# Optimization experiments

Measured on AMD Instinct MI355X. Metric: run time of the kernel, lower is better.

## Reference

```python
import math
import jax, jax.numpy as jnp
import numpy as np

B, N, F, K = 4, 4096, 128, 32
EPS = 1e-8  # tsl.epsilon
TEMP0, TEMP_DECAY = 1.0, 0.99995


def setup_inputs() -> dict:
    key = jax.random.key(0)
    k1, k2, k3, k4 = jax.random.split(key, 4)
    emb = jax.random.normal(k1, (B, N, F), dtype=jnp.float32)
    adj = jax.random.uniform(k2, (B, N, N), dtype=jnp.float32)
    logits_param = jax.random.normal(k3, (N, K), dtype=jnp.float32)
    u = jax.random.uniform(k4, (B, N, K), dtype=jnp.float32, minval=1e-9, maxval=1.0)
    gumbel_noise = -jnp.log(-jnp.log(u))
    return {"emb": emb, "adj": adj, "logits_param": logits_param, "gumbel_noise": gumbel_noise}


def reference(emb, adj, logits_param, gumbel_noise):
    # temp decays on each get_temp() call in training mode (called twice per forward)
    t1 = max(TEMP0 * TEMP_DECAY, 0.05)
    t2 = max(t1 * TEMP_DECAY, 0.05)

    # ---- gumbel-softmax hard sample with straight-through estimator ----
    y_soft = jax.nn.softmax(logits_param[None] / t1 + gumbel_noise, axis=-1)  # [B,N,K]
    y_hard = jax.nn.one_hot(jnp.argmax(y_soft, axis=-1), K, dtype=y_soft.dtype)
    s_sample = jax.lax.stop_gradient(y_hard - y_soft) + y_soft + EPS  # [B,N,K]

    # ---- soft assignment for regularizers (unbatched [N,K]) ----
    s_soft = jax.nn.softmax(logits_param / t2, axis=-1)  # [N,K]

    # mincut_num = trace(s^T A s) per batch, without forming [K,K]
    As = jnp.einsum('bnm,mk->bnk', adj, s_soft)            # [B,N,K]
    mincut_num = jnp.einsum('nk,bnk->b', s_soft, As)       # [B]
    # mincut_den = trace(s^T D s): D is diag(deg) -> O(N*K) instead of diag_embed
    d_flat = adj.sum(axis=-1)                              # [B,N]
    mincut_den = jnp.einsum('bn,nk,nk->b', d_flat, s_soft, s_soft)
    mincut_loss = -jnp.mean(mincut_num / mincut_den)

    ss = s_soft.T @ s_soft                                 # [K,K]
    ortho_loss = jnp.linalg.norm(ss / jnp.linalg.norm(ss) - jnp.eye(K, dtype=ss.dtype) / math.sqrt(K))

    # ---- pooling ----
    out_emb = jnp.einsum('bnk,bnf->bkf', s_sample, emb)    # [B,K,F]
    As2 = jnp.einsum('bnm,bml->bnl', adj, s_sample)        # [B,N,K]
    out_adj = jnp.einsum('bnk,bnl->bkl', s_sample, As2)    # [B,K,K]

    out_adj = out_adj * (1.0 - jnp.eye(K, dtype=out_adj.dtype))  # zero diagonal
    d = jnp.sqrt(out_adj.sum(axis=-1, keepdims=True)) + EPS
    out_adj = out_adj / d / jnp.swapaxes(d, -1, -2)

    return out_emb, out_adj, s_sample, mincut_loss, ortho_loss
```

## Files before the change

kernel.cpp:

```cpp
#include <hip/hip_runtime.h>
#include <hip/hip_bf16.h>
#include <math.h>

#define B_ 4
#define N_ 4096
#define F_ 128
#define K_ 32
#define EPS_ 1e-8f

typedef __attribute__((ext_vector_type(8))) __bf16 bf16x8;
typedef __attribute__((ext_vector_type(4))) float f32x4;

#define WS_SSOFT 0
#define WS_SQ    131072
#define WS_SS    135168
#define WS_NUM   136192
#define WS_DEN   136196
#define WS_OADJ  136200
#define WS_WF    140296
#define WS_H     664584

__global__ void k_ssoft(const float* __restrict__ logits, float* __restrict__ s_soft,
                        float* __restrict__ sq, float* __restrict__ ss, float t2) {
  __shared__ float sl[64][33];
  int t = threadIdx.x;
  int rowbase = blockIdx.x * 64;
  if (t < 64) {
    int n = rowbase + t;
    float z[32];
    float mx = -1e30f;
    for (int k = 0; k < 32; ++k) { z[k] = logits[n*32+k] / t2; mx = fmaxf(mx, z[k]); }
    float s = 0.f;
    for (int k = 0; k < 32; ++k) { z[k] = expf(z[k]-mx); s += z[k]; }
    float sqa = 0.f;
    for (int k = 0; k < 32; ++k) {
      float v = z[k] / s;
      s_soft[n*32+k] = v;
      sl[t][k] = v;
      sqa += v*v;
    }
    sq[n] = sqa;
  }
  __syncthreads();
  for (int pp = 0; pp < 4; ++pp) {
    int p = pp*256 + t;
    int k = p >> 5, l = p & 31;
    float a = 0.f;
    for (int r = 0; r < 64; ++r) a += sl[r][k]*sl[r][l];
    atomicAdd(&ss[p], a);
  }
}

__global__ void k_gumbel(const float* __restrict__ logits, const float* __restrict__ gum,
                         float* __restrict__ s_sample, int* __restrict__ h, float t1) {
  int i = blockIdx.x*256 + threadIdx.x;
  int n = i & (N_-1);
  float z[32];
  float mx = -1e30f;
  for (int k = 0; k < 32; ++k) { z[k] = logits[n*32+k]/t1 + gum[(size_t)i*32+k]; mx = fmaxf(mx, z[k]); }
  float s = 0.f;
  for (int k = 0; k < 32; ++k) { z[k] = expf(z[k]-mx); s += z[k]; }
  int am = 0; float best = -1.f;
  for (int k = 0; k < 32; ++k) { z[k] = z[k]/s; if (z[k] > best) { best = z[k]; am = k; } }
  for (int k = 0; k < 32; ++k) {
    float yh = (k==am) ? 1.f : 0.f;
    s_sample[(size_t)i*32+k] = (yh - z[k]) + z[k] + EPS_;
  }
  h[i] = am;
}

__global__ void k_wfrag(const float* __restrict__ s_soft, const int* __restrict__ h,
                        bf16x8* __restrict__ wf) {
  int i = blockIdx.x*256 + threadIdx.x;
  int lane = i & 63;
  int c = (i >> 6) & 3;
  int tt = (i >> 8) & 127;
  int b = i >> 15;
  int col = c*16 + (lane & 15);
  int m0 = tt*32 + (lane >> 4)*8;
  bf16x8 v;
  if (col < 32) {
    for (int j = 0; j < 8; ++j) v[j] = (__bf16)s_soft[(m0+j)*32 + col];
  } else {
    int cc = col - 32;
    for (int j = 0; j < 8; ++j) v[j] = (__bf16)((h[b*N_ + m0 + j] == cc) ? 1.f : 0.f);
  }
  wf[i] = v;
}

__launch_bounds__(256, 2)
__global__ void k_gemm(const float* __restrict__ adj, const bf16x8* __restrict__ wf,
                       const float* __restrict__ s_soft, const float* __restrict__ sq,
                       const int* __restrict__ h, float* __restrict__ num,
                       float* __restrict__ den, float* __restrict__ oadj) {
  __shared__ float oal[1024];
  __shared__ float rn[4], rd[4];
  int t = threadIdx.x;
  int w = t >> 6, l = t & 63;
  int lr = l & 15, lhi = l >> 4;
  int bid = blockIdx.x;
  int sp = bid & 3, r = (bid >> 2) & 31, b = bid >> 7;

  for (int i = t; i < 1024; i += 256) oal[i] = 0.f;
  __syncthreads();

  int row0 = r*128 + w*32;
  int m0 = sp*1024;
  const float* adjb = adj + (size_t)b*N_*N_;
  const float* arow0 = adjb + (size_t)(row0 + lr)*N_ + m0 + lhi*8;
  const float* arow1 = arow0 + (size_t)16*N_;
  const bf16x8* wfb = wf + ((size_t)b*128 + (m0 >> 5))*256 + l;

  f32x4 acc[2][4];
  for (int i = 0; i < 2; ++i)
    for (int j = 0; j < 4; ++j) acc[i][j] = (f32x4){0.f,0.f,0.f,0.f};

  for (int t32 = 0; t32 < 32; ++t32) {
    float4 a0 = *(const float4*)(arow0);
    float4 a1 = *(const float4*)(arow0 + 4);
    float4 a2 = *(const float4*)(arow1);
    float4 a3 = *(const float4*)(arow1 + 4);
    bf16x8 bf0 = wfb[0], bf1 = wfb[64], bf2 = wfb[128], bf3 = wfb[192];
    bf16x8 af0, af1;
    af0[0]=(__bf16)a0.x; af0[1]=(__bf16)a0.y; af0[2]=(__bf16)a0.z; af0[3]=(__bf16)a0.w;
    af0[4]=(__bf16)a1.x; af0[5]=(__bf16)a1.y; af0[6]=(__bf16)a1.z; af0[7]=(__bf16)a1.w;
    af1[0]=(__bf16)a2.x; af1[1]=(__bf16)a2.y; af1[2]=(__bf16)a2.z; af1[3]=(__bf16)a2.w;
    af1[4]=(__bf16)a3.x; af1[5]=(__bf16)a3.y; af1[6]=(__bf16)a3.z; af1[7]=(__bf16)a3.w;
    acc[0][0] = __builtin_amdgcn_mfma_f32_16x16x32_bf16(af0, bf0, acc[0][0], 0, 0, 0);
    acc[0][1] = __builtin_amdgcn_mfma_f32_16x16x32_bf16(af0, bf1, acc[0][1], 0, 0, 0);
    acc[0][2] = __builtin_amdgcn_mfma_f32_16x16x32_bf16(af0, bf2, acc[0][2], 0, 0, 0);
    acc[0][3] = __builtin_amdgcn_mfma_f32_16x16x32_bf16(af0, bf3, acc[0][3], 0, 0, 0);
    acc[1][0] = __builtin_amdgcn_mfma_f32_16x16x32_bf16(af1, bf0, acc[1][0], 0, 0, 0);
    acc[1][1] = __builtin_amdgcn_mfma_f32_16x16x32_bf16(af1, bf1, acc[1][1], 0, 0, 0);
    acc[1][2] = __builtin_amdgcn_mfma_f32_16x16x32_bf16(af1, bf2, acc[1][2], 0, 0, 0);
    acc[1][3] = __builtin_amdgcn_mfma_f32_16x16x32_bf16(af1, bf3, acc[1][3], 0, 0, 0);
    arow0 += 32; arow1 += 32; wfb += 256;
  }

  float numacc = 0.f, denacc = 0.f;
  for (int rt = 0; rt < 2; ++rt) {
    int rbase = row0 + rt*16 + lhi*4;
    for (int i = 0; i < 4; ++i) {
      int row = rbase + i;
      float sqv = sq[row];
      int hv = h[b*N_ + row];
      numacc += acc[rt][0][i] * s_soft[row*32 + lr];
      numacc += acc[rt][1][i] * s_soft[row*32 + 16 + lr];
      float v2 = acc[rt][2][i], v3 = acc[rt][3][i];
      denacc += (v2 + v3) * sqv;
      atomicAdd(&oal[hv*32 + lr], v2);
      atomicAdd(&oal[hv*32 + 16 + lr], v3);
    }
  }
  for (int off = 32; off; off >>= 1) {
    numacc += __shfl_down(numacc, off);
    denacc += __shfl_down(denacc, off);
  }
  if (l == 0) { rn[w] = numacc; rd[w] = denacc; }
  __syncthreads();
  if (t == 0) {
    atomicAdd(&num[b], rn[0]+rn[1]+rn[2]+rn[3]);
    atomicAdd(&den[b], rd[0]+rd[1]+rd[2]+rd[3]);
  }
  for (int i = t; i < 1024; i += 256) atomicAdd(&oadj[b*1024 + i], oal[i]);
}

__global__ void k_outemb(const float* __restrict__ emb, const int* __restrict__ h,
                         float* __restrict__ out_emb) {
  __shared__ float accl[32*128];
  int t = threadIdx.x;
  for (int i = t; i < 4096; i += 256) accl[i] = 0.f;
  __syncthreads();
  int b = blockIdx.x >> 5;
  int n0 = (blockIdx.x & 31) * 128;
  int f = t & 127, rr = t >> 7;
  for (int it = 0; it < 64; ++it) {
    int n = n0 + it*2 + rr;
    float v = emb[((size_t)b*N_ + n)*F_ + f];
    int hv = h[b*N_ + n];
    atomicAdd(&accl[hv*128 + f], v);
  }
  __syncthreads();
  for (int i = t; i < 4096; i += 256) atomicAdd(&out_emb[b*4096 + i], accl[i]);
}

__global__ void k_final(const float* __restrict__ num, const float* __restrict__ den,
                        const float* __restrict__ oadj, const float* __restrict__ ss,
                        float* __restrict__ dout) {
  __shared__ float dsh[128];
  __shared__ float red[256];
  int t = threadIdx.x;
  if (t < 128) {
    int b = t >> 5, k = t & 31;
    float s = 0.f;
    for (int l = 0; l < 32; ++l) if (l != k) s += oadj[b*1024 + k*32 + l];
    dsh[t] = sqrtf(s) + EPS_;
  }
  __syncthreads();
  for (int i = t; i < 4096; i += 256) {
    int b = i >> 10, k = (i >> 5) & 31, l = i & 31;
    float v = (k == l) ? 0.f : oadj[i] / (dsh[b*32+k] * dsh[b*32+l]);
    dout[16384 + i] = v;
  }
  float a = 0.f;
  for (int i = t; i < 1024; i += 256) { float v = ss[i]; a += v*v; }
  red[t] = a; __syncthreads();
  for (int s2 = 128; s2; s2 >>= 1) { if (t < s2) red[t] += red[t+s2]; __syncthreads(); }
  float fro = sqrtf(red[0]);
  __syncthreads();
  float c = 0.f;
  float inv = 1.f / fro;
  float dk = (float)(1.0 / sqrt(32.0));
  for (int i = t; i < 1024; i += 256) {
    int k = i >> 5, l = i & 31;
    float v = ss[i]*inv - ((k == l) ? dk : 0.f);
    c += v*v;
  }
  red[t] = c; __syncthreads();
  for (int s2 = 128; s2; s2 >>= 1) { if (t < s2) red[t] += red[t+s2]; __syncthreads(); }
  if (t == 0) {
    dout[544769] = sqrtf(red[0]);
    float s = 0.f;
    for (int b = 0; b < 4; ++b) s += num[b]/den[b];
    dout[544768] = -s*0.25f;
  }
}

extern "C" void kernel_launch(void* const* d_in, const int* in_sizes, int n_in,
                              void* d_out, int out_size, void* d_ws, size_t ws_size,
                              hipStream_t stream) {
  const float* emb    = (const float*)d_in[0];
  const float* adj    = (const float*)d_in[1];
  const float* logits = (const float*)d_in[2];
  const float* gum    = (const float*)d_in[3];
  float* out = (float*)d_out;
  float* ws  = (float*)d_ws;

  float t1 = 0.99995f;
  float t2 = (float)(0.99995 * 0.99995);

  float* s_soft = ws + WS_SSOFT;
  float* sq     = ws + WS_SQ;
  float* ss     = ws + WS_SS;
  float* num    = ws + WS_NUM;
  float* den    = ws + WS_DEN;
  float* oadj   = ws + WS_OADJ;
  bf16x8* wf    = (bf16x8*)(ws + WS_WF);
  int* hbuf     = (int*)(ws + WS_H);

  hipMemsetAsync(ss, 0, 5128 * sizeof(float), stream);
  hipMemsetAsync(out, 0, 16384 * sizeof(float), stream);

  k_ssoft <<<64, 256, 0, stream>>>(logits, s_soft, sq, ss, t2);
  k_gumbel<<<64, 256, 0, stream>>>(logits, gum, out + 20480, hbuf, t1);
  k_wfrag <<<512, 256, 0, stream>>>(s_soft, hbuf, wf);
  k_gemm  <<<512, 256, 0, stream>>>(adj, wf, s_soft, sq, hbuf, num, den, oadj);
  k_outemb<<<128, 256, 0, stream>>>(emb, hbuf, out);
  k_final <<<1, 256, 0, stream>>>(num, den, oadj, ss, out);
}
```

Baseline: 473.4 us.

## Split GEMM K-dimension finer, double-buffer adj loads, replace atomics with partial reductions

The adjacency GEMM now splits the reduction dimension eight ways instead of four (1024 blocks), raises launch bounds to four blocks per SM, and software-pipelines the adj loads with a two-stage register double buffer using nontemporal loads. Global atomics for num/den, out_adj and out_emb are replaced by per-block partial outputs that a new reduce kernel and the final kernel sum. This is meant to increase memory-level parallelism on the bandwidth-bound 268MB adj stream and to remove atomic contention and the output memset. The cost is extra workspace traffic for the partials and one more kernel launch.

```diff
diff --git a/kernel.cpp b/kernel.cpp
--- a/kernel.cpp
+++ b/kernel.cpp
@@ -11,14 +11,15 @@
 typedef __attribute__((ext_vector_type(8))) __bf16 bf16x8;
 typedef __attribute__((ext_vector_type(4))) float f32x4;
 
-#define WS_SSOFT 0
-#define WS_SQ    131072
-#define WS_SS    135168
-#define WS_NUM   136192
-#define WS_DEN   136196
-#define WS_OADJ  136200
-#define WS_WF    140296
-#define WS_H     664584
+#define WS_SSOFT   0
+#define WS_SQ      131072
+#define WS_SS      135168
+#define WS_WF      136192
+#define WS_OADJP   660480
+#define WS_NUMDEN  1709056
+#define WS_PEMB    1711104
+#define WS_OADJ    2235392
+#define WS_H       2239488
 
 __global__ void k_ssoft(const float* __restrict__ logits, float* __restrict__ s_soft,
                         float* __restrict__ sq, float* __restrict__ ss, float t2) {
@@ -88,68 +89,81 @@
   wf[i] = v;
 }
 
-__launch_bounds__(256, 2)
+#define CVT8(dst, va, vb) { dst[0]=(__bf16)va[0]; dst[1]=(__bf16)va[1]; dst[2]=(__bf16)va[2]; dst[3]=(__bf16)va[3]; \
+                            dst[4]=(__bf16)vb[0]; dst[5]=(__bf16)vb[1]; dst[6]=(__bf16)vb[2]; dst[7]=(__bf16)vb[3]; }
+
+#define MFMA8(A0,A1,A2,A3,W0,W1,W2,W3) { \
+  bf16x8 af0, af1; CVT8(af0, A0, A1); CVT8(af1, A2, A3); \
+  acc00 = __builtin_amdgcn_mfma_f32_16x16x32_bf16(af0, W0, acc00, 0, 0, 0); \
+  acc01 = __builtin_amdgcn_mfma_f32_16x16x32_bf16(af0, W1, acc01, 0, 0, 0); \
+  acc02 = __builtin_amdgcn_mfma_f32_16x16x32_bf16(af0, W2, acc02, 0, 0, 0); \
+  acc03 = __builtin_amdgcn_mfma_f32_16x16x32_bf16(af0, W3, acc03, 0, 0, 0); \
+  acc10 = __builtin_amdgcn_mfma_f32_16x16x32_bf16(af1, W0, acc10, 0, 0, 0); \
+  acc11 = __builtin_amdgcn_mfma_f32_16x16x32_bf16(af1, W1, acc11, 0, 0, 0); \
+  acc12 = __builtin_amdgcn_mfma_f32_16x16x32_bf16(af1, W2, acc12, 0, 0, 0); \
+  acc13 = __builtin_amdgcn_mfma_f32_16x16x32_bf16(af1, W3, acc13, 0, 0, 0); }
+
+#define NT(p) __builtin_nontemporal_load((const f32x4*)(p))
+
+__launch_bounds__(256, 4)
 __global__ void k_gemm(const float* __restrict__ adj, const bf16x8* __restrict__ wf,
                        const float* __restrict__ s_soft, const float* __restrict__ sq,
-                       const int* __restrict__ h, float* __restrict__ num,
-                       float* __restrict__ den, float* __restrict__ oadj) {
+                       const int* __restrict__ h, float* __restrict__ numden_p,
+                       float* __restrict__ oadjp) {
   __shared__ float oal[1024];
   __shared__ float rn[4], rd[4];
   int t = threadIdx.x;
   int w = t >> 6, l = t & 63;
   int lr = l & 15, lhi = l >> 4;
   int bid = blockIdx.x;
-  int sp = bid & 3, r = (bid >> 2) & 31, b = bid >> 7;
+  int sp = bid & 7, r = (bid >> 3) & 31, b = bid >> 8;
 
   for (int i = t; i < 1024; i += 256) oal[i] = 0.f;
   __syncthreads();
 
   int row0 = r*128 + w*32;
-  int m0 = sp*1024;
-  const float* adjb = adj + (size_t)b*N_*N_;
-  const float* arow0 = adjb + (size_t)(row0 + lr)*N_ + m0 + lhi*8;
-  const float* arow1 = arow0 + (size_t)16*N_;
-  const bf16x8* wfb = wf + ((size_t)b*128 + (m0 >> 5))*256 + l;
-
-  f32x4 acc[2][4];
-  for (int i = 0; i < 2; ++i)
-    for (int j = 0; j < 4; ++j) acc[i][j] = (f32x4){0.f,0.f,0.f,0.f};
-
-  for (int t32 = 0; t32 < 32; ++t32) {
-    float4 a0 = *(const float4*)(arow0);
-    float4 a1 = *(const float4*)(arow0 + 4);
-    float4 a2 = *(const float4*)(arow1);
-    float4 a3 = *(const float4*)(arow1 + 4);
-    bf16x8 bf0 = wfb[0], bf1 = wfb[64], bf2 = wfb[128], bf3 = wfb[192];
-    bf16x8 af0, af1;
-    af0[0]=(__bf16)a0.x; af0[1]=(__bf16)a0.y; af0[2]=(__bf16)a0.z; af0[3]=(__bf16)a0.w;
-    af0[4]=(__bf16)a1.x; af0[5]=(__bf16)a1.y; af0[6]=(__bf16)a1.z; af0[7]=(__bf16)a1.w;
-    af1[0]=(__bf16)a2.x; af1[1]=(__bf16)a2.y; af1[2]=(__bf16)a2.z; af1[3]=(__bf16)a2.w;
-    af1[4]=(__bf16)a3.x; af1[5]=(__bf16)a3.y; af1[6]=(__bf16)a3.z; af1[7]=(__bf16)a3.w;
-    acc[0][0] = __builtin_amdgcn_mfma_f32_16x16x32_bf16(af0, bf0, acc[0][0], 0, 0, 0);
-    acc[0][1] = __builtin_amdgcn_mfma_f32_16x16x32_bf16(af0, bf1, acc[0][1], 0, 0, 0);
-    acc[0][2] = __builtin_amdgcn_mfma_f32_16x16x32_bf16(af0, bf2, acc[0][2], 0, 0, 0);
-    acc[0][3] = __builtin_amdgcn_mfma_f32_16x16x32_bf16(af0, bf3, acc[0][3], 0, 0, 0);
-    acc[1][0] = __builtin_amdgcn_mfma_f32_16x16x32_bf16(af1, bf0, acc[1][0], 0, 0, 0);
-    acc[1][1] = __builtin_amdgcn_mfma_f32_16x16x32_bf16(af1, bf1, acc[1][1], 0, 0, 0);
-    acc[1][2] = __builtin_amdgcn_mfma_f32_16x16x32_bf16(af1, bf2, acc[1][2], 0, 0, 0);
-    acc[1][3] = __builtin_amdgcn_mfma_f32_16x16x32_bf16(af1, bf3, acc[1][3], 0, 0, 0);
-    arow0 += 32; arow1 += 32; wfb += 256;
+  int m0 = sp*512;
+  const float* pa0 = adj + (size_t)b*N_*N_ + (size_t)(row0 + lr)*N_ + m0 + lhi*8;
+  const float* pa1 = pa0 + (size_t)16*N_;
+  const bf16x8* pw = wf + ((size_t)b*128 + (m0 >> 5))*256 + l;
+
+  f32x4 acc00 = {0,0,0,0}, acc01 = {0,0,0,0}, acc02 = {0,0,0,0}, acc03 = {0,0,0,0};
+  f32x4 acc10 = {0,0,0,0}, acc11 = {0,0,0,0}, acc12 = {0,0,0,0}, acc13 = {0,0,0,0};
+
+  f32x4 xa0 = NT(pa0), xa1 = NT(pa0+4), xa2 = NT(pa1), xa3 = NT(pa1+4);
+  f32x4 ya0, ya1, ya2, ya3;
+  bf16x8 w0, w1, w2, w3;
+
+  #pragma unroll 1
+  for (int it = 0; it < 16; it += 2) {
+    ya0 = NT(pa0+32); ya1 = NT(pa0+36); ya2 = NT(pa1+32); ya3 = NT(pa1+36);
+    w0 = pw[0]; w1 = pw[64]; w2 = pw[128]; w3 = pw[192];
+    MFMA8(xa0, xa1, xa2, xa3, w0, w1, w2, w3);
+    pw += 256;
+    if (it + 2 < 16) { xa0 = NT(pa0+64); xa1 = NT(pa0+68); xa2 = NT(pa1+64); xa3 = NT(pa1+68); }
+    w0 = pw[0]; w1 = pw[64]; w2 = pw[128]; w3 = pw[192];
+    MFMA8(ya0, ya1, ya2, ya3, w0, w1, w2, w3);
+    pw += 256;
+    pa0 += 64; pa1 += 64;
   }
 
   float numacc = 0.f, denacc = 0.f;
-  for (int rt = 0; rt < 2; ++rt) {
-    int rbase = row0 + rt*16 + lhi*4;
-    for (int i = 0; i < 4; ++i) {
-      int row = rbase + i;
-      float sqv = sq[row];
-      int hv = h[b*N_ + row];
-      numacc += acc[rt][0][i] * s_soft[row*32 + lr];
-      numacc += acc[rt][1][i] * s_soft[row*32 + 16 + lr];
-      float v2 = acc[rt][2][i], v3 = acc[rt][3][i];
-      denacc += (v2 + v3) * sqv;
-      atomicAdd(&oal[hv*32 + lr], v2);
-      atomicAdd(&oal[hv*32 + 16 + lr], v3);
+  {
+    f32x4 a0s[2] = {acc00, acc10}, a1s[2] = {acc01, acc11};
+    f32x4 a2s[2] = {acc02, acc12}, a3s[2] = {acc03, acc13};
+    for (int rt = 0; rt < 2; ++rt) {
+      int rbase = row0 + rt*16 + lhi*4;
+      for (int i = 0; i < 4; ++i) {
+        int row = rbase + i;
+        float sqv = sq[row];
+        int hv = h[b*N_ + row];
+        numacc += a0s[rt][i] * s_soft[row*32 + lr];
+        numacc += a1s[rt][i] * s_soft[row*32 + 16 + lr];
+        float v2 = a2s[rt][i], v3 = a3s[rt][i];
+        denacc += (v2 + v3) * sqv;
+        atomicAdd(&oal[hv*32 + lr], v2);
+        atomicAdd(&oal[hv*32 + 16 + lr], v3);
+      }
     }
   }
   for (int off = 32; off; off >>= 1) {
@@ -159,14 +173,14 @@
   if (l == 0) { rn[w] = numacc; rd[w] = denacc; }
   __syncthreads();
   if (t == 0) {
-    atomicAdd(&num[b], rn[0]+rn[1]+rn[2]+rn[3]);
-    atomicAdd(&den[b], rd[0]+rd[1]+rd[2]+rd[3]);
-  }
-  for (int i = t; i < 1024; i += 256) atomicAdd(&oadj[b*1024 + i], oal[i]);
+    numden_p[bid] = rn[0]+rn[1]+rn[2]+rn[3];
+    numden_p[1024 + bid] = rd[0]+rd[1]+rd[2]+rd[3];
+  }
+  for (int i = t; i < 1024; i += 256) oadjp[(size_t)bid*1024 + i] = oal[i];
 }
 
 __global__ void k_outemb(const float* __restrict__ emb, const int* __restrict__ h,
-                         float* __restrict__ out_emb) {
+                         float* __restrict__ pemb) {
   __shared__ float accl[32*128];
   int t = threadIdx.x;
   for (int i = t; i < 4096; i += 256) accl[i] = 0.f;
@@ -181,20 +195,48 @@
     atomicAdd(&accl[hv*128 + f], v);
   }
   __syncthreads();
-  for (int i = t; i < 4096; i += 256) atomicAdd(&out_emb[b*4096 + i], accl[i]);
-}
-
-__global__ void k_final(const float* __restrict__ num, const float* __restrict__ den,
-                        const float* __restrict__ oadj, const float* __restrict__ ss,
-                        float* __restrict__ dout) {
+  for (int i = t; i < 4096; i += 256) pemb[(size_t)blockIdx.x*4096 + i] = accl[i];
+}
+
+__global__ void k_reduce(const float* __restrict__ oadjp, const float* __restrict__ pemb,
+                         float* __restrict__ oadj, float* __restrict__ out_emb) {
+  int blk = blockIdx.x;
+  if (blk < 16) {
+    int i = blk*256 + threadIdx.x;
+    int b = i >> 10, ii = i & 1023;
+    float s = 0.f;
+    const float* p = oadjp + (size_t)(b*256)*1024 + ii;
+    for (int j = 0; j < 256; ++j) s += p[(size_t)j*1024];
+    oadj[i] = s;
+  } else {
+    int i = (blk-16)*256 + threadIdx.x;
+    int b = i >> 12, ii = i & 4095;
+    float s = 0.f;
+    const float* p = pemb + (size_t)(b*32)*4096 + ii;
+    for (int j = 0; j < 32; ++j) s += p[(size_t)j*4096];
+    out_emb[i] = s;
+  }
+}
+
+__global__ void k_final(const float* __restrict__ numden_p, const float* __restrict__ oadj,
+                        const float* __restrict__ ss, float* __restrict__ dout) {
   __shared__ float dsh[128];
   __shared__ float red[256];
+  __shared__ float nd[8];
   int t = threadIdx.x;
-  if (t < 128) {
-    int b = t >> 5, k = t & 31;
+  if (t < 8) {
+    int b = t & 3;
+    const float* p = numden_p + (t >> 2)*1024 + b*256;
+    float s = 0.f;
+    for (int j = 0; j < 256; ++j) s += p[j];
+    nd[t] = s;
+  }
+  if (t >= 64 && t < 192) {
+    int i = t - 64;
+    int b = i >> 5, k = i & 31;
     float s = 0.f;
     for (int l = 0; l < 32; ++l) if (l != k) s += oadj[b*1024 + k*32 + l];
-    dsh[t] = sqrtf(s) + EPS_;
+    dsh[i] = sqrtf(s) + EPS_;
   }
   __syncthreads();
   for (int i = t; i < 4096; i += 256) {
@@ -221,7 +263,7 @@
   if (t == 0) {
     dout[544769] = sqrtf(red[0]);
     float s = 0.f;
-    for (int b = 0; b < 4; ++b) s += num[b]/den[b];
+    for (int b = 0; b < 4; ++b) s += nd[b] / nd[4+b];
     dout[544768] = -s*0.25f;
   }
 }
@@ -242,19 +284,20 @@
   float* s_soft = ws + WS_SSOFT;
   float* sq     = ws + WS_SQ;
   float* ss     = ws + WS_SS;
-  float* num    = ws + WS_NUM;
-  float* den    = ws + WS_DEN;
+  bf16x8* wf    = (bf16x8*)(ws + WS_WF);
+  float* oadjp  = ws + WS_OADJP;
+  float* ndp    = ws + WS_NUMDEN;
+  float* pemb   = ws + WS_PEMB;
   float* oadj   = ws + WS_OADJ;
-  bf16x8* wf    = (bf16x8*)(ws + WS_WF);
   int* hbuf     = (int*)(ws + WS_H);
 
-  hipMemsetAsync(ss, 0, 5128 * sizeof(float), stream);
-  hipMemsetAsync(out, 0, 16384 * sizeof(float), stream);
+  (void)hipMemsetAsync(ss, 0, 1024 * sizeof(float), stream);
 
   k_ssoft <<<64, 256, 0, stream>>>(logits, s_soft, sq, ss, t2);
   k_gumbel<<<64, 256, 0, stream>>>(logits, gum, out + 20480, hbuf, t1);
   k_wfrag <<<512, 256, 0, stream>>>(s_soft, hbuf, wf);
-  k_gemm  <<<512, 256, 0, stream>>>(adj, wf, s_soft, sq, hbuf, num, den, oadj);
-  k_outemb<<<128, 256, 0, stream>>>(emb, hbuf, out);
-  k_final <<<1, 256, 0, stream>>>(num, den, oadj, ss, out);
-}
+  k_gemm  <<<1024, 256, 0, stream>>>(adj, wf, s_soft, sq, hbuf, ndp, oadjp);
+  k_outemb<<<128, 256, 0, stream>>>(emb, hbuf, pemb);
+  k_reduce<<<80, 256, 0, stream>>>(oadjp, pemb, oadj, out);
+  k_final <<<1, 256, 0, stream>>>(ndp, oadj, ss, out);
+}
```

Result: faster. 444.8 us (-6.0%).
